# Optimization experiments

Measured on AMD Instinct MI355X. Metric: run time of the kernel, lower is better.

The kernel has to match this reference:

```python
import jax, jax.numpy as jnp
import numpy as np

C = 64       # class_number (from json groups)
D = 256      # out_dimension = predicted.shape[1]
N = 262144   # batch size


def setup_inputs() -> dict:
    key = jax.random.key(0)
    k1, k2, k3, k4 = jax.random.split(key, 4)
    predicted = jax.random.normal(k1, (N, D), dtype=jnp.float32)
    target = jax.random.randint(k2, (N,), 0, C)
    centroids = jax.random.normal(k3, (C, D), dtype=jnp.float32)
    # accumulated per-class distance sums are nonnegative (sqrt is applied)
    distances = jax.random.uniform(k4, (C, 1), dtype=jnp.float32) * float(N)
    # count = bincount(target) as the torch module accumulates; clamp >= 1
    ones = jnp.ones((N,), jnp.float32)
    count = jnp.maximum(jax.ops.segment_sum(ones, target, num_segments=C), 1.0)[:, None]
    # build_class_weight_matrix: single group containing every label -> all 1.5
    class_weights = jnp.full((C, C), 1.5, dtype=jnp.float32)
    return dict(predicted=predicted, centroids=centroids, distances=distances,
                count=count, class_weights=class_weights, target=target)


def reference(predicted, centroids, distances, count, class_weights, target):
    # === calculate_loss path (epoch % 3 == 2) ===
    C_ = centroids.shape[0]
    sel_counts = count[target]            # [N,1] gather
    sel_centroids = centroids[target]     # [N,D] gather
    pr = predicted / sel_counts           # [N,D]
    cent_new = centroids.at[target].add(pr)                 # scatter-add
    vec = jnp.linalg.norm(sel_centroids - pr, axis=1)       # [N]
    s = distances.at[target].add(vec[:, None])              # scatter-add [C,1]
    s = jnp.sqrt(s) / count                                 # [C,1]
    # cdist(cent_new, cent_new, p=2) via the norm trick
    sq = jnp.sum(cent_new * cent_new, axis=1)               # [C]
    d2 = jnp.maximum(sq[:, None] + sq[None, :] - 2.0 * (cent_new @ cent_new.T), 0.0)
    mask = ~jnp.eye(C_, dtype=bool)
    m = jnp.sqrt(jnp.where(mask, d2, 1.0))                  # safe off-diagonal sqrt
    S = s + s.T                                             # s[i] + s[j], [C,C]
    term = jnp.where(mask, class_weights * S / m, 0.0)
    sum_ = jnp.sum(term)
    loss = sum_ / C_ * (C_ - 1)
    return loss + jnp.sum(jnp.abs(cent_new)) / 1000000.0
```

## Files before the change

kernel.cpp:

```cpp
#include <hip/hip_runtime.h>
#include <math.h>

#define NROWS 262144
#define DIM   256
#define NC    64
#define CD    (NC*DIM)
#define NBLK  512

#define OFF_CENT   0
#define OFF_SF     16384
#define OFF_ABS    16448
#define OFF_PAIR   16704
#define OFF_SPART  16768
#define OFF_PART   49536

typedef short  bf16x8 __attribute__((ext_vector_type(8)));
typedef float  f32x16 __attribute__((ext_vector_type(16)));

#define DPP_ADD(v, ctrl) \
    ((v) + __int_as_float(__builtin_amdgcn_update_dpp(0, __float_as_int(v), (ctrl), 0xf, 0xf, true)))

__device__ __forceinline__ float dpp_sum64(float v) {
    v = DPP_ADD(v, 0x111);
    v = DPP_ADD(v, 0x112);
    v = DPP_ADD(v, 0x114);
    v = DPP_ADD(v, 0x118);
    v = DPP_ADD(v, 0x142);
    v = DPP_ADD(v, 0x143);
    return v;
}

__device__ __forceinline__ unsigned int bf16rne2(float lo, float hi) {
    unsigned int ul = __float_as_uint(lo);
    ul = (ul + 0x7FFFu + ((ul >> 16) & 1u)) >> 16;
    unsigned int uh = __float_as_uint(hi);
    uh = (uh + 0x7FFFu + ((uh >> 16) & 1u)) & 0xFFFF0000u;
    return ul | uh;
}
__device__ __forceinline__ unsigned short bf16rne1(float v) {
    unsigned int x = __float_as_uint(v);
    return (unsigned short)((x + 0x7FFFu + ((x >> 16) & 1u)) >> 16);
}
__device__ __forceinline__ float bflo(unsigned int u) { return __uint_as_float(u << 16); }
__device__ __forceinline__ float bfhi(unsigned int u) { return __uint_as_float(u & 0xFFFF0000u); }
__device__ __forceinline__ float bfup(unsigned short u) { return __uint_as_float(((unsigned int)u) << 16); }

__device__ __forceinline__ void do_mfma_chunk(const unsigned short* pb,
                                              const int* tgts, int rbase,
                                              int lane, int d0,
                                              f32x16& a0r, f32x16& a1r)
{
    const int g8  = (lane >> 5) << 3;
    const int cA  = lane & 31;
    const int cB  = 32 + cA;
    const int col = d0 + cA;
    #pragma unroll
    for (int ks = 0; ks < 4; ++ks) {
        const int rA = rbase + ks * 16 + g8;
        const int t0 = tgts[rA+0], t1 = tgts[rA+1], t2 = tgts[rA+2], t3 = tgts[rA+3];
        const int t4 = tgts[rA+4], t5 = tgts[rA+5], t6 = tgts[rA+6], t7 = tgts[rA+7];
        union { unsigned int u[4]; bf16x8 v; } A0, A1, B;
        A0.u[0] = ((t0==cA)?0x3F80u:0u) | (((t1==cA)?0x3F80u:0u) << 16);
        A0.u[1] = ((t2==cA)?0x3F80u:0u) | (((t3==cA)?0x3F80u:0u) << 16);
        A0.u[2] = ((t4==cA)?0x3F80u:0u) | (((t5==cA)?0x3F80u:0u) << 16);
        A0.u[3] = ((t6==cA)?0x3F80u:0u) | (((t7==cA)?0x3F80u:0u) << 16);
        A1.u[0] = ((t0==cB)?0x3F80u:0u) | (((t1==cB)?0x3F80u:0u) << 16);
        A1.u[1] = ((t2==cB)?0x3F80u:0u) | (((t3==cB)?0x3F80u:0u) << 16);
        A1.u[2] = ((t4==cB)?0x3F80u:0u) | (((t5==cB)?0x3F80u:0u) << 16);
        A1.u[3] = ((t6==cB)?0x3F80u:0u) | (((t7==cB)?0x3F80u:0u) << 16);
        const int kr = ks * 16 + g8;
        #pragma unroll
        for (int p = 0; p < 4; ++p) {
            const unsigned int lo = pb[(kr + 2*p    ) * 256 + col];
            const unsigned int hi = pb[(kr + 2*p + 1) * 256 + col];
            B.u[p] = lo | (hi << 16);
        }
        a0r = __builtin_amdgcn_mfma_f32_32x32x16_bf16(A0.v, B.v, a0r, 0, 0, 0);
        a1r = __builtin_amdgcn_mfma_f32_32x32x16_bf16(A1.v, B.v, a1r, 0, 0, 0);
    }
}

__global__ __launch_bounds__(512, 4)
void k_main(const float* __restrict__ pred, const float* __restrict__ cent,
            const float* __restrict__ count, const int* __restrict__ tgt,
            float* __restrict__ ws)
{
    __shared__ unsigned short pbf[64 * 256];
    __shared__ unsigned short cbf[NC * 256];
    __shared__ int   tgt_s[512];
    __shared__ float inv_s[64];
    __shared__ float vec_s[512];
    __shared__ float sw_s[8][64];

    const int tid  = threadIdx.x;
    const int w    = tid >> 6;
    const int lane = tid & 63;
    const int base = blockIdx.x * 512;

    tgt_s[tid] = tgt[base + tid];
    if (tid < 64) inv_s[tid] = 1.0f / count[tid];
    {
        const float2* c2 = (const float2*)cent;
        unsigned int* cb32 = (unsigned int*)cbf;
        #pragma unroll
        for (int i = 0; i < 16; ++i) {
            const int o = i * 512 + tid;
            const float2 cf = c2[o];
            cb32[o] = bf16rne2(cf.x, cf.y);
        }
    }
    __syncthreads();

    const float4* pred4 = (const float4*)pred;
    const int d0 = w * 32;

    f32x16 acc0 = {};
    f32x16 acc1 = {};

    #pragma unroll 1
    for (int ch = 0; ch < 8; ++ch) {
        const size_t gr = (size_t)(base + ch * 64) * 64 + lane;
        float4 p0 = pred4[gr + (size_t)( 0 + w) * 64];
        float4 p1 = pred4[gr + (size_t)( 8 + w) * 64];
        float4 p2 = pred4[gr + (size_t)(16 + w) * 64];
        float4 p3 = pred4[gr + (size_t)(24 + w) * 64];
        float4 p4 = pred4[gr + (size_t)(32 + w) * 64];
        float4 p5 = pred4[gr + (size_t)(40 + w) * 64];
        float4 p6 = pred4[gr + (size_t)(48 + w) * 64];
        float4 p7 = pred4[gr + (size_t)(56 + w) * 64];

#define ROW(pp, i)                                                             \
        {                                                                      \
            const int rc = 8*(i) + w;                                          \
            const int r  = ch * 64 + rc;                                       \
            const int c  = tgt_s[r];                                           \
            const float iv = inv_s[c];                                         \
            const uint2 cu = *(const uint2*)&cbf[c * 256 + lane * 4];          \
            const float dx = bflo(cu.x) - pp.x * iv;                           \
            const float dy = bfhi(cu.x) - pp.y * iv;                           \
            const float dz = bflo(cu.y) - pp.z * iv;                           \
            const float dw = bfhi(cu.y) - pp.w * iv;                           \
            float ss = dx*dx + dy*dy + dz*dz + dw*dw;                          \
            ss = dpp_sum64(ss);                                                \
            if (lane == 63) vec_s[r] = sqrtf(ss);                              \
            *(uint2*)&pbf[rc * 256 + lane * 4] =                               \
                make_uint2(bf16rne2(pp.x, pp.y), bf16rne2(pp.z, pp.w));        \
        }
        ROW(p0, 0) ROW(p1, 1) ROW(p2, 2) ROW(p3, 3)
        ROW(p4, 4) ROW(p5, 5) ROW(p6, 6) ROW(p7, 7)
#undef ROW
        __syncthreads();
        do_mfma_chunk(pbf, tgt_s, ch * 64, lane, d0, acc0, acc1);
        __syncthreads();
    }

    unsigned short* pp = (unsigned short*)(ws + OFF_PART) + (size_t)blockIdx.x * CD;
    const int dim = d0 + (lane & 31);
    #pragma unroll
    for (int reg = 0; reg < 16; ++reg) {
        const int crow = (reg & 3) + 8 * (reg >> 2) + 4 * (lane >> 5);
        pp[(     crow) * 256 + dim] = bf16rne1(acc0[reg]);
        pp[(32 + crow) * 256 + dim] = bf16rne1(acc1[reg]);
    }

    {
        const float vv = vec_s[w * 64 + lane];
        const int   cc = tgt_s[w * 64 + lane];
        float accs = 0.f;
        for (int k = 0; k < NC; ++k) {
            float sel = (cc == k) ? vv : 0.f;
            sel = dpp_sum64(sel);
            const float tot = __shfl(sel, 63, 64);
            accs += (lane == k) ? tot : 0.f;
        }
        sw_s[w][lane] = accs;
    }
    __syncthreads();
    if (w == 0) {
        float s = 0.f;
        #pragma unroll
        for (int q = 0; q < 8; ++q) s += sw_s[q][lane];
        ws[OFF_SPART + blockIdx.x * 64 + lane] = s;
    }
}

__global__ __launch_bounds__(256)
void k_redbuild(const float* __restrict__ cent, const float* __restrict__ count,
                const float* __restrict__ dist, float* __restrict__ ws)
{
    const int b = blockIdx.x, t = threadIdx.x;
    __shared__ float red[4][64];
    if (b < 256) {
        const int e  = b * 64 + (t & 63);
        const int ps = t >> 6;
        const unsigned short* pp = (const unsigned short*)(ws + OFF_PART) + e;
        float s = 0.f;
        const int pstart = ps * 128;
        #pragma unroll 8
        for (int p = pstart; p < pstart + 128; ++p) s += bfup(pp[(size_t)p * CD]);
        red[ps][t & 63] = s;
        __syncthreads();
        if (t < 64) {
            const float tot = red[0][t] + red[1][t] + red[2][t] + red[3][t];
            const int o = b * 64 + t;
            const int c = o >> 8;
            const float inv = 1.0f / count[c];
            const float val = cent[o] + tot * inv;
            ws[OFF_CENT + o] = val;
            float a = fabsf(val);
            a = dpp_sum64(a);
            if (t == 63) ws[OFF_ABS + b] = a;
        }
    } else {
        const int c = t & 63, g = t >> 6;
        float s = 0.f;
        const int pstart = g * 128;
        #pragma unroll 8
        for (int p = pstart; p < pstart + 128; ++p) s += ws[OFF_SPART + p * 64 + c];
        red[g][c] = s;
        __syncthreads();
        if (t < 64) {
            const float sv = red[0][t] + red[1][t] + red[2][t] + red[3][t];
            ws[OFF_SF + t] = sqrtf(dist[t] + sv) / count[t];
        }
    }
}

__global__ __launch_bounds__(256)
void k3_pairs(const float* __restrict__ cw, float* __restrict__ ws)
{
    const int i    = blockIdx.x;
    const int tid  = threadIdx.x;
    const int lane = tid & 63;
    const int w    = tid >> 6;
    const float4* c4 = (const float4*)(ws + OFF_CENT);
    const float*  sf = ws + OFF_SF;

    float4 ci = c4[i * 64 + lane];
    float  si = sf[i];
    float acc = 0.f;
    for (int j = w; j < NC; j += 4) {
        if (j == i) continue;
        float4 cj = c4[j * 64 + lane];
        float dx = ci.x - cj.x, dy = ci.y - cj.y;
        float dz = ci.z - cj.z, dw = ci.w - cj.w;
        float ss = dx*dx + dy*dy + dz*dz + dw*dw;
        #pragma unroll
        for (int o = 32; o > 0; o >>= 1) ss += __shfl_xor(ss, o, 64);
        acc += cw[i * NC + j] * (si + sf[j]) / sqrtf(ss);
    }
    __shared__ float wsum[4];
    if (lane == 0) wsum[w] = acc;
    __syncthreads();
    if (tid == 0) ws[OFF_PAIR + i] = wsum[0] + wsum[1] + wsum[2] + wsum[3];
}

__global__ __launch_bounds__(256)
void k4_final(const float* __restrict__ ws, float* __restrict__ out)
{
    const int t = threadIdx.x;
    float a = ws[OFF_ABS + t];
    float p = (t < 64) ? ws[OFF_PAIR + t] : 0.f;
    #pragma unroll
    for (int o = 32; o > 0; o >>= 1) {
        a += __shfl_xor(a, o, 64);
        p += __shfl_xor(p, o, 64);
    }
    __shared__ float ra[4], rp[4];
    if ((t & 63) == 0) { ra[t >> 6] = a; rp[t >> 6] = p; }
    __syncthreads();
    if (t == 0) {
        float ps = rp[0] + rp[1] + rp[2] + rp[3];
        float as = ra[0] + ra[1] + ra[2] + ra[3];
        out[0] = ps / 64.0f * 63.0f + as * 1e-6f;
    }
}

extern "C" void kernel_launch(void* const* d_in, const int* in_sizes, int n_in,
                              void* d_out, int out_size, void* d_ws, size_t ws_size,
                              hipStream_t stream)
{
    const float* pred  = (const float*)d_in[0];
    const float* cent  = (const float*)d_in[1];
    const float* dist  = (const float*)d_in[2];
    const float* count = (const float*)d_in[3];
    const float* cw    = (const float*)d_in[4];
    const int*   tgt   = (const int*)d_in[5];
    float* ws  = (float*)d_ws;
    float* out = (float*)d_out;

    k_main    <<<NBLK, 512, 0, stream>>>(pred, cent, count, tgt, ws);
    k_redbuild<<<257,  256, 0, stream>>>(cent, count, dist, ws);
    k3_pairs  <<<NC,   256, 0, stream>>>(cw, ws);
    k4_final  <<<1,    256, 0, stream>>>(ws, out);
}
```

Measured before the change: 82.97 us.

## Fuse four kernels into one cooperative kernel with grid syncs

```diff
diff --git a/kernel.cpp b/kernel.cpp
--- a/kernel.cpp
+++ b/kernel.cpp
@@ -1,5 +1,8 @@
 #include <hip/hip_runtime.h>
+#include <hip/hip_cooperative_groups.h>
 #include <math.h>
+
+namespace cg = cooperative_groups;
 
 #define NROWS 262144
 #define DIM   256
@@ -8,11 +11,11 @@
 #define NBLK  512
 
 #define OFF_CENT   0
-#define OFF_SF     16384
-#define OFF_ABS    16448
-#define OFF_PAIR   16704
-#define OFF_SPART  16768
-#define OFF_PART   49536
+#define OFF_ABS    16384
+#define OFF_PAIR   16896
+#define OFF_SPART  16960
+#define OFF_SST2   49728
+#define OFF_PART   50752
 
 typedef short  bf16x8 __attribute__((ext_vector_type(8)));
 typedef float  f32x16 __attribute__((ext_vector_type(16)));
@@ -81,198 +84,213 @@
 }
 
 __global__ __launch_bounds__(512, 4)
-void k_main(const float* __restrict__ pred, const float* __restrict__ cent,
-            const float* __restrict__ count, const int* __restrict__ tgt,
-            float* __restrict__ ws)
+void k_fused(const float* __restrict__ pred, const float* __restrict__ cent,
+             const float* __restrict__ count, const float* __restrict__ dist,
+             const float* __restrict__ cw, const int* __restrict__ tgt,
+             float* __restrict__ ws, float* __restrict__ out, int phase)
 {
+    cg::grid_group grid = cg::this_grid();
+
     __shared__ unsigned short pbf[64 * 256];
     __shared__ unsigned short cbf[NC * 256];
     __shared__ int   tgt_s[512];
     __shared__ float inv_s[64];
     __shared__ float vec_s[512];
     __shared__ float sw_s[8][64];
+    __shared__ float red2[16][32];
+    __shared__ float sred[8][64];
 
     const int tid  = threadIdx.x;
     const int w    = tid >> 6;
     const int lane = tid & 63;
-    const int base = blockIdx.x * 512;
-
-    tgt_s[tid] = tgt[base + tid];
-    if (tid < 64) inv_s[tid] = 1.0f / count[tid];
-    {
-        const float2* c2 = (const float2*)cent;
-        unsigned int* cb32 = (unsigned int*)cbf;
+
+    if (phase <= 0) {
+        const int base = blockIdx.x * 512;
+        tgt_s[tid] = tgt[base + tid];
+        if (tid < 64) inv_s[tid] = 1.0f / count[tid];
+        {
+            const float2* c2 = (const float2*)cent;
+            unsigned int* cb32 = (unsigned int*)cbf;
+            #pragma unroll
+            for (int i = 0; i < 16; ++i) {
+                const int o = i * 512 + tid;
+                const float2 cf = c2[o];
+                cb32[o] = bf16rne2(cf.x, cf.y);
+            }
+        }
+        __syncthreads();
+
+        const float4* pred4 = (const float4*)pred;
+        const int d0 = w * 32;
+
+        f32x16 acc0 = {};
+        f32x16 acc1 = {};
+
+        #pragma unroll 1
+        for (int ch = 0; ch < 8; ++ch) {
+            const size_t gr = (size_t)(base + ch * 64) * 64 + lane;
+            float4 p0 = pred4[gr + (size_t)( 0 + w) * 64];
+            float4 p1 = pred4[gr + (size_t)( 8 + w) * 64];
+            float4 p2 = pred4[gr + (size_t)(16 + w) * 64];
+            float4 p3 = pred4[gr + (size_t)(24 + w) * 64];
+            float4 p4 = pred4[gr + (size_t)(32 + w) * 64];
+            float4 p5 = pred4[gr + (size_t)(40 + w) * 64];
+            float4 p6 = pred4[gr + (size_t)(48 + w) * 64];
+            float4 p7 = pred4[gr + (size_t)(56 + w) * 64];
+
+#define ROW(pp, i)                                                             \
+            {                                                                  \
+                const int rc = 8*(i) + w;                                      \
+                const int r  = ch * 64 + rc;                                   \
+                const int c  = tgt_s[r];                                       \
+                const float iv = inv_s[c];                                     \
+                const uint2 cu = *(const uint2*)&cbf[c * 256 + lane * 4];      \
+                const float dx = bflo(cu.x) - pp.x * iv;                       \
+                const float dy = bfhi(cu.x) - pp.y * iv;                       \
+                const float dz = bflo(cu.y) - pp.z * iv;                       \
+                const float dw = bfhi(cu.y) - pp.w * iv;                       \
+                float ss = dx*dx + dy*dy + dz*dz + dw*dw;                      \
+                ss = dpp_sum64(ss);                                            \
+                if (lane == 63) vec_s[r] = sqrtf(ss);                          \
+                *(uint2*)&pbf[rc * 256 + lane * 4] =                           \
+                    make_uint2(bf16rne2(pp.x, pp.y), bf16rne2(pp.z, pp.w));    \
+            }
+            ROW(p0, 0) ROW(p1, 1) ROW(p2, 2) ROW(p3, 3)
+            ROW(p4, 4) ROW(p5, 5) ROW(p6, 6) ROW(p7, 7)
+#undef ROW
+            __syncthreads();
+            do_mfma_chunk(pbf, tgt_s, ch * 64, lane, d0, acc0, acc1);
+            __syncthreads();
+        }
+
+        unsigned short* pp = (unsigned short*)(ws + OFF_PART) + (size_t)blockIdx.x * CD;
+        const int dim = d0 + (lane & 31);
         #pragma unroll
-        for (int i = 0; i < 16; ++i) {
-            const int o = i * 512 + tid;
-            const float2 cf = c2[o];
-            cb32[o] = bf16rne2(cf.x, cf.y);
-        }
-    }
-    __syncthreads();
-
-    const float4* pred4 = (const float4*)pred;
-    const int d0 = w * 32;
-
-    f32x16 acc0 = {};
-    f32x16 acc1 = {};
-
-    #pragma unroll 1
-    for (int ch = 0; ch < 8; ++ch) {
-        const size_t gr = (size_t)(base + ch * 64) * 64 + lane;
-        float4 p0 = pred4[gr + (size_t)( 0 + w) * 64];
-        float4 p1 = pred4[gr + (size_t)( 8 + w) * 64];
-        float4 p2 = pred4[gr + (size_t)(16 + w) * 64];
-        float4 p3 = pred4[gr + (size_t)(24 + w) * 64];
-        float4 p4 = pred4[gr + (size_t)(32 + w) * 64];
-        float4 p5 = pred4[gr + (size_t)(40 + w) * 64];
-        float4 p6 = pred4[gr + (size_t)(48 + w) * 64];
-        float4 p7 = pred4[gr + (size_t)(56 + w) * 64];
-
-#define ROW(pp, i)                                                             \
-        {                                                                      \
-            const int rc = 8*(i) + w;                                          \
-            const int r  = ch * 64 + rc;                                       \
-            const int c  = tgt_s[r];                                           \
-            const float iv = inv_s[c];                                         \
-            const uint2 cu = *(const uint2*)&cbf[c * 256 + lane * 4];          \
-            const float dx = bflo(cu.x) - pp.x * iv;                           \
-            const float dy = bfhi(cu.x) - pp.y * iv;                           \
-            const float dz = bflo(cu.y) - pp.z * iv;                           \
-            const float dw = bfhi(cu.y) - pp.w * iv;                           \
-            float ss = dx*dx + dy*dy + dz*dz + dw*dw;                          \
-            ss = dpp_sum64(ss);                                                \
-            if (lane == 63) vec_s[r] = sqrtf(ss);                              \
-            *(uint2*)&pbf[rc * 256 + lane * 4] =                               \
-                make_uint2(bf16rne2(pp.x, pp.y), bf16rne2(pp.z, pp.w));        \
-        }
-        ROW(p0, 0) ROW(p1, 1) ROW(p2, 2) ROW(p3, 3)
-        ROW(p4, 4) ROW(p5, 5) ROW(p6, 6) ROW(p7, 7)
-#undef ROW
-        __syncthreads();
-        do_mfma_chunk(pbf, tgt_s, ch * 64, lane, d0, acc0, acc1);
-        __syncthreads();
-    }
-
-    unsigned short* pp = (unsigned short*)(ws + OFF_PART) + (size_t)blockIdx.x * CD;
-    const int dim = d0 + (lane & 31);
-    #pragma unroll
-    for (int reg = 0; reg < 16; ++reg) {
-        const int crow = (reg & 3) + 8 * (reg >> 2) + 4 * (lane >> 5);
-        pp[(     crow) * 256 + dim] = bf16rne1(acc0[reg]);
-        pp[(32 + crow) * 256 + dim] = bf16rne1(acc1[reg]);
-    }
-
-    {
-        const float vv = vec_s[w * 64 + lane];
-        const int   cc = tgt_s[w * 64 + lane];
-        float accs = 0.f;
-        for (int k = 0; k < NC; ++k) {
-            float sel = (cc == k) ? vv : 0.f;
-            sel = dpp_sum64(sel);
-            const float tot = __shfl(sel, 63, 64);
-            accs += (lane == k) ? tot : 0.f;
-        }
-        sw_s[w][lane] = accs;
-    }
-    __syncthreads();
-    if (w == 0) {
+        for (int reg = 0; reg < 16; ++reg) {
+            const int crow = (reg & 3) + 8 * (reg >> 2) + 4 * (lane >> 5);
+            pp[(     crow) * 256 + dim] = bf16rne1(acc0[reg]);
+            pp[(32 + crow) * 256 + dim] = bf16rne1(acc1[reg]);
+        }
+
+        {
+            const float vv = vec_s[w * 64 + lane];
+            const int   cc = tgt_s[w * 64 + lane];
+            float accs = 0.f;
+            for (int k = 0; k < NC; ++k) {
+                float sel = (cc == k) ? vv : 0.f;
+                sel = dpp_sum64(sel);
+                const float tot = __shfl(sel, 63, 64);
+                accs += (lane == k) ? tot : 0.f;
+            }
+            sw_s[w][lane] = accs;
+        }
+        __syncthreads();
+        if (w == 0) {
+            float s = 0.f;
+            #pragma unroll
+            for (int q = 0; q < 8; ++q) s += sw_s[q][lane];
+            ws[OFF_SPART + blockIdx.x * 64 + lane] = s;
+        }
+    }
+
+    if (phase < 0) grid.sync();
+
+    if (phase < 0 || phase == 1) {
+        const int b  = blockIdx.x;
+        const int eo = tid & 31;
+        const int g  = tid >> 5;
+        const int e  = b * 32 + eo;
+        const unsigned short* pp = (const unsigned short*)(ws + OFF_PART);
         float s = 0.f;
-        #pragma unroll
-        for (int q = 0; q < 8; ++q) s += sw_s[q][lane];
-        ws[OFF_SPART + blockIdx.x * 64 + lane] = s;
-    }
-}
-
-__global__ __launch_bounds__(256)
-void k_redbuild(const float* __restrict__ cent, const float* __restrict__ count,
-                const float* __restrict__ dist, float* __restrict__ ws)
-{
-    const int b = blockIdx.x, t = threadIdx.x;
-    __shared__ float red[4][64];
-    if (b < 256) {
-        const int e  = b * 64 + (t & 63);
-        const int ps = t >> 6;
-        const unsigned short* pp = (const unsigned short*)(ws + OFF_PART) + e;
-        float s = 0.f;
-        const int pstart = ps * 128;
+        const int p0 = g * 32;
         #pragma unroll 8
-        for (int p = pstart; p < pstart + 128; ++p) s += bfup(pp[(size_t)p * CD]);
-        red[ps][t & 63] = s;
-        __syncthreads();
-        if (t < 64) {
-            const float tot = red[0][t] + red[1][t] + red[2][t] + red[3][t];
-            const int o = b * 64 + t;
-            const int c = o >> 8;
-            const float inv = 1.0f / count[c];
-            const float val = cent[o] + tot * inv;
-            ws[OFF_CENT + o] = val;
-            float a = fabsf(val);
+        for (int p = p0; p < p0 + 32; ++p) s += bfup(pp[(size_t)p * CD + e]);
+        red2[g][eo] = s;
+        __syncthreads();
+        if (tid < 32) {
+            float tot = 0.f;
+            #pragma unroll
+            for (int q = 0; q < 16; ++q) tot += red2[q][tid];
+            const int e2 = b * 32 + tid;
+            const int c  = e2 >> 8;
+            const float val = cent[e2] + tot / count[c];
+            ws[OFF_CENT + e2] = val;
+            vec_s[tid] = fabsf(val);
+        }
+        __syncthreads();
+        if (tid < 64) {
+            float a = (tid < 32) ? vec_s[tid] : 0.f;
             a = dpp_sum64(a);
-            if (t == 63) ws[OFF_ABS + b] = a;
-        }
-    } else {
-        const int c = t & 63, g = t >> 6;
-        float s = 0.f;
-        const int pstart = g * 128;
-        #pragma unroll 8
-        for (int p = pstart; p < pstart + 128; ++p) s += ws[OFF_SPART + p * 64 + c];
-        red[g][c] = s;
-        __syncthreads();
-        if (t < 64) {
-            const float sv = red[0][t] + red[1][t] + red[2][t] + red[3][t];
-            ws[OFF_SF + t] = sqrtf(dist[t] + sv) / count[t];
-        }
-    }
-}
-
-__global__ __launch_bounds__(256)
-void k3_pairs(const float* __restrict__ cw, float* __restrict__ ws)
-{
-    const int i    = blockIdx.x;
-    const int tid  = threadIdx.x;
-    const int lane = tid & 63;
-    const int w    = tid >> 6;
-    const float4* c4 = (const float4*)(ws + OFF_CENT);
-    const float*  sf = ws + OFF_SF;
-
-    float4 ci = c4[i * 64 + lane];
-    float  si = sf[i];
-    float acc = 0.f;
-    for (int j = w; j < NC; j += 4) {
-        if (j == i) continue;
-        float4 cj = c4[j * 64 + lane];
-        float dx = ci.x - cj.x, dy = ci.y - cj.y;
-        float dz = ci.z - cj.z, dw = ci.w - cj.w;
-        float ss = dx*dx + dy*dy + dz*dz + dw*dw;
-        #pragma unroll
-        for (int o = 32; o > 0; o >>= 1) ss += __shfl_xor(ss, o, 64);
-        acc += cw[i * NC + j] * (si + sf[j]) / sqrtf(ss);
-    }
-    __shared__ float wsum[4];
-    if (lane == 0) wsum[w] = acc;
-    __syncthreads();
-    if (tid == 0) ws[OFF_PAIR + i] = wsum[0] + wsum[1] + wsum[2] + wsum[3];
-}
-
-__global__ __launch_bounds__(256)
-void k4_final(const float* __restrict__ ws, float* __restrict__ out)
-{
-    const int t = threadIdx.x;
-    float a = ws[OFF_ABS + t];
-    float p = (t < 64) ? ws[OFF_PAIR + t] : 0.f;
-    #pragma unroll
-    for (int o = 32; o > 0; o >>= 1) {
-        a += __shfl_xor(a, o, 64);
-        p += __shfl_xor(p, o, 64);
-    }
-    __shared__ float ra[4], rp[4];
-    if ((t & 63) == 0) { ra[t >> 6] = a; rp[t >> 6] = p; }
-    __syncthreads();
-    if (t == 0) {
-        float ps = rp[0] + rp[1] + rp[2] + rp[3];
-        float as = ra[0] + ra[1] + ra[2] + ra[3];
-        out[0] = ps / 64.0f * 63.0f + as * 1e-6f;
+            if (tid == 63) ws[OFF_ABS + b] = a;
+        }
+        if (b >= 496) {
+            const int q  = b - 496;
+            const int c  = tid & 63;
+            const int rw = tid >> 6;
+            float s2 = 0.f;
+            #pragma unroll
+            for (int i = 0; i < 4; ++i)
+                s2 += ws[OFF_SPART + (q * 32 + rw * 4 + i) * 64 + c];
+            sred[rw][c] = s2;
+            __syncthreads();
+            if (tid < 64) {
+                float sv = 0.f;
+                #pragma unroll
+                for (int r = 0; r < 8; ++r) sv += sred[r][tid];
+                ws[OFF_SST2 + q * 64 + tid] = sv;
+            }
+        }
+    }
+
+    if (phase < 0) grid.sync();
+
+    if ((phase < 0 || phase == 2) && blockIdx.x < 64) {
+        const int i = blockIdx.x;
+        if (tid < 64) {
+            float sv = 0.f;
+            #pragma unroll
+            for (int q = 0; q < 16; ++q) sv += ws[OFF_SST2 + q * 64 + tid];
+            inv_s[tid] = sqrtf(dist[tid] + sv) / count[tid];
+        }
+        __syncthreads();
+        const float4* c4 = (const float4*)(ws + OFF_CENT);
+        const float si = inv_s[i];
+        const float4 ci = c4[i * 64 + lane];
+        float acc = 0.f;
+        for (int j = w; j < NC; j += 8) {
+            if (j == i) continue;
+            const float4 cj = c4[j * 64 + lane];
+            const float dx = ci.x - cj.x, dy = ci.y - cj.y;
+            const float dz = ci.z - cj.z, dw = ci.w - cj.w;
+            float ss = dx*dx + dy*dy + dz*dz + dw*dw;
+            ss = dpp_sum64(ss);
+            if (lane == 63) acc += cw[i * NC + j] * (si + inv_s[j]) / sqrtf(ss);
+        }
+        if (lane == 63) sw_s[w][0] = acc;
+        __syncthreads();
+        if (tid == 0) {
+            float ps = 0.f;
+            #pragma unroll
+            for (int q = 0; q < 8; ++q) ps += sw_s[q][0];
+            ws[OFF_PAIR + i] = ps;
+        }
+    }
+
+    if (phase < 0) grid.sync();
+
+    if ((phase < 0 || phase == 3) && blockIdx.x == 0) {
+        float a = ws[OFF_ABS + tid];
+        float p = (tid < 64) ? ws[OFF_PAIR + tid] : 0.f;
+        a = dpp_sum64(a);
+        p = dpp_sum64(p);
+        if (lane == 63) { sw_s[w][0] = a; sw_s[w][1] = p; }
+        __syncthreads();
+        if (tid == 0) {
+            float as = 0.f, ps = 0.f;
+            #pragma unroll
+            for (int q = 0; q < 8; ++q) { as += sw_s[q][0]; ps += sw_s[q][1]; }
+            out[0] = ps / 64.0f * 63.0f + as * 1e-6f;
+        }
     }
 }
 
@@ -289,8 +307,17 @@
     float* ws  = (float*)d_ws;
     float* out = (float*)d_out;
 
-    k_main    <<<NBLK, 512, 0, stream>>>(pred, cent, count, tgt, ws);
-    k_redbuild<<<257,  256, 0, stream>>>(cent, count, dist, ws);
-    k3_pairs  <<<NC,   256, 0, stream>>>(cw, ws);
-    k4_final  <<<1,    256, 0, stream>>>(ws, out);
-}
+    int phase_all = -1;
+    void* args[] = { (void*)&pred, (void*)&cent, (void*)&count, (void*)&dist,
+                     (void*)&cw, (void*)&tgt, (void*)&ws, (void*)&out,
+                     (void*)&phase_all };
+    hipError_t err = hipLaunchCooperativeKernel((const void*)k_fused,
+                                                dim3(NBLK), dim3(512),
+                                                args, 0, stream);
+    if (err != hipSuccess) {
+        k_fused<<<NBLK, 512, 0, stream>>>(pred, cent, count, dist, cw, tgt, ws, out, 0);
+        k_fused<<<NBLK, 512, 0, stream>>>(pred, cent, count, dist, cw, tgt, ws, out, 1);
+        k_fused<<<64,   512, 0, stream>>>(pred, cent, count, dist, cw, tgt, ws, out, 2);
+        k_fused<<<1,    512, 0, stream>>>(pred, cent, count, dist, cw, tgt, ws, out, 3);
+    }
+}
```

New measurement: 241.4 us. 2.91x slower.
